# Performance work log

Hardware: AMD Instinct MI355X
Metric: run time of the kernel (lower is better)

## Reference

```python
import jax, jax.numpy as jnp
import numpy as np

N_NODES = 100000
N_EDGES = 800000
D = 128
BN_EPS = 1e-5


def setup_inputs() -> dict:
    key = jax.random.key(0)
    k1, k2, k3 = jax.random.split(key, 3)
    x = jax.random.normal(k1, (N_NODES, D), dtype=jnp.float32)
    # Glorot-ish init for the GCN weight
    W = jax.random.normal(k2, (D, D), dtype=jnp.float32) * (1.0 / np.sqrt(D))
    b = jnp.zeros((D,), dtype=jnp.float32)
    gamma = jnp.ones((D,), dtype=jnp.float32)
    beta = jnp.zeros((D,), dtype=jnp.float32)
    edge_index = jax.random.randint(k3, (2, N_EDGES), 0, N_NODES, dtype=jnp.int64)
    return {"x": x, "W": W, "b": b, "gamma": gamma, "beta": beta,
            "edge_index": edge_index}


def reference(x, W, b, gamma, beta, edge_index):
    N = x.shape[0]
    # --- GCNConv: add self-loops, symmetric degree normalization ---
    loop = jnp.arange(N, dtype=edge_index.dtype)
    src = jnp.concatenate([edge_index[0], loop])
    dst = jnp.concatenate([edge_index[1], loop])
    deg = jax.ops.segment_sum(jnp.ones_like(dst, dtype=x.dtype), dst,
                              num_segments=N)
    deg_inv_sqrt = jax.lax.rsqrt(deg)  # deg >= 1 thanks to self-loops
    norm = deg_inv_sqrt[src] * deg_inv_sqrt[dst]  # [E+N]

    h = x @ W  # [N, D] linear transform before propagation
    msg = h[src] * norm[:, None]  # gather + edge scaling, [E+N, D]
    agg = jax.ops.segment_sum(msg, dst, num_segments=N) + b  # scatter-add

    # --- BatchNorm1d (training-mode batch statistics, biased variance) ---
    mean = jnp.mean(agg, axis=0)
    var = jnp.mean(jnp.square(agg - mean), axis=0)
    y = gamma * (agg - mean) * jax.lax.rsqrt(var + BN_EPS) + beta

    # --- ReLU (dropout is identity in deterministic reference) ---
    return jax.nn.relu(y)
```

## Files before the change

### kernel.cpp

```cpp
#include <hip/hip_runtime.h>


#define N_NODES 100000
#define N_EDGES 800000
#define D 128
#define BN_EPS 1e-5f
#define SCAN_NB 98

__global__ void detect_i64(const unsigned int* ei, int* flag) {
    __shared__ int nonzero;
    if (threadIdx.x == 0) nonzero = 0;
    __syncthreads();
    int local = 0;
    for (int i = threadIdx.x; i < 2048; i += 256)
        if (ei[2 * i + 1] != 0u) local = 1;
    if (local) atomicOr(&nonzero, 1);
    __syncthreads();
    if (threadIdx.x == 0) *flag = (nonzero == 0) ? 1 : 0;
}

__device__ __forceinline__ int edge_at(const void* ei, int is64, long long pos) {
    if (is64) return (int)((const long long*)ei)[pos];
    return ((const int*)ei)[pos];
}

__global__ void count_deg_i(const void* ei, const int* __restrict__ flag,
                            int* __restrict__ deg) {
    int is64 = *flag;
    for (int i = blockIdx.x * blockDim.x + threadIdx.x; i < N_EDGES;
         i += gridDim.x * blockDim.x) {
        int d = edge_at(ei, is64, (long long)N_EDGES + i);
        atomicAdd(&deg[d], 1);
    }
}

__global__ __launch_bounds__(256) void scan1(const int* __restrict__ deg,
                                             int* __restrict__ rp,
                                             int* __restrict__ bsum) {
    __shared__ int wsum[4];
    int tid = threadIdx.x;
    int base = blockIdx.x * 1024;
    int v[4];
#pragma unroll
    for (int i = 0; i < 4; ++i) {
        int idx = base + tid * 4 + i;
        v[i] = (idx < N_NODES) ? deg[idx] : 0;
    }
    int tsum = v[0] + v[1] + v[2] + v[3];
    int lane = tid & 63;
    int incl = tsum;
#pragma unroll
    for (int off = 1; off < 64; off <<= 1) {
        int n = __shfl_up(incl, off, 64);
        if (lane >= off) incl += n;
    }
    int wid = tid >> 6;
    if (lane == 63) wsum[wid] = incl;
    __syncthreads();
    int woff = 0;
    for (int w = 0; w < wid; ++w) woff += wsum[w];
    int run = woff + incl - tsum;
#pragma unroll
    for (int i = 0; i < 4; ++i) {
        int idx = base + tid * 4 + i;
        if (idx < N_NODES) rp[idx] = run;
        run += v[i];
    }
    if (tid == 255) bsum[blockIdx.x] = woff + incl;
}

__global__ void scan2(int* __restrict__ bsum, int* __restrict__ rp) {
    __shared__ int s[128];
    int t = threadIdx.x;
    if (t < SCAN_NB) s[t] = bsum[t];
    __syncthreads();
    if (t == 0) {
        int run = 0;
        for (int i = 0; i < SCAN_NB; ++i) { int x = s[i]; s[i] = run; run += x; }
        rp[N_NODES] = N_EDGES;
    }
    __syncthreads();
    if (t < SCAN_NB) bsum[t] = s[t];
}

__global__ void scan3(int* __restrict__ rp, const int* __restrict__ bsum,
                      int* __restrict__ fp, const int* __restrict__ deg,
                      float* __restrict__ dis) {
    int idx = blockIdx.x * 256 + threadIdx.x;
    if (idx < N_NODES) {
        int v = rp[idx] + bsum[idx >> 10];
        rp[idx] = v;
        fp[idx] = v;
        dis[idx] = rsqrtf((float)deg[idx] + 1.0f);
    }
}

__global__ void fill_csr(const void* ei, const int* __restrict__ flag,
                         int* __restrict__ fp, int* __restrict__ ebuf) {
    int is64 = *flag;
    for (int e = blockIdx.x * blockDim.x + threadIdx.x; e < N_EDGES;
         e += gridDim.x * blockDim.x) {
        int s = edge_at(ei, is64, e);
        int d = edge_at(ei, is64, (long long)N_EDGES + e);
        int pos = atomicAdd(&fp[d], 1);
        ebuf[pos] = s;
    }
}

__global__ __launch_bounds__(256) void gather_x(const int* __restrict__ rp,
                                                const int* __restrict__ ebuf,
                                                const float* __restrict__ dis,
                                                const float* __restrict__ x,
                                                float* __restrict__ aggx) {
    int lane = threadIdx.x & 63;
    int wid = threadIdx.x >> 6;
    const float2* x2 = (const float2*)x;
    for (int node = blockIdx.x * 4 + wid; node < N_NODES;
         node += gridDim.x * 4) {
        int beg = rp[node], end = rp[node + 1];
        float dd = dis[node];
        float a0 = 0.f, a1 = 0.f;
        for (int j = beg; j < end; ++j) {
            int s = ebuf[j];
            float coef = dis[s] * dd;
            float2 v = x2[(size_t)s * 64 + lane];
            a0 = fmaf(v.x, coef, a0);
            a1 = fmaf(v.y, coef, a1);
        }
        float2 xv = x2[(size_t)node * 64 + lane];
        float c2 = dd * dd;
        a0 = fmaf(xv.x, c2, a0);
        a1 = fmaf(xv.y, c2, a1);
        ((float2*)aggx)[(size_t)node * 64 + lane] = make_float2(a0, a1);
    }
}

__global__ __launch_bounds__(256) void gemm_stats(float* __restrict__ ax,
                                                  const float* __restrict__ Wm,
                                                  float* __restrict__ colsum,
                                                  float* __restrict__ colsumsq) {
    __shared__ float As[64 * 128];
    __shared__ float Ws[64 * 128];
    int tid = threadIdx.x;
    int row0 = blockIdx.x * 64;

    const float4* a4 = (const float4*)ax;
    float4* A4 = (float4*)As;
#pragma unroll
    for (int i = 0; i < 8; ++i) {
        int idx = tid + i * 256;
        int r = idx >> 5;
        int gr = row0 + r;
        A4[idx] = (gr < N_NODES) ? a4[(size_t)gr * 32 + (idx & 31)]
                                 : make_float4(0.f, 0.f, 0.f, 0.f);
    }

    int tx = tid & 31;
    int ty = tid >> 5;
    float acc[8][4] = {};
    const float* Arow = &As[ty * 8 * 128];
    const float4* W4 = (const float4*)Wm;
    float4* Ws4 = (float4*)Ws;

    for (int kc = 0; kc < 128; kc += 64) {
        __syncthreads();
#pragma unroll
        for (int i = 0; i < 8; ++i) {
            int idx = tid + i * 256;
            Ws4[idx] = W4[kc * 32 + idx];
        }
        __syncthreads();
#pragma unroll 8
        for (int k = 0; k < 64; ++k) {
            float4 w = ((const float4*)&Ws[k * 128])[tx];
#pragma unroll
            for (int r = 0; r < 8; ++r) {
                float a = Arow[r * 128 + kc + k];
                acc[r][0] = fmaf(a, w.x, acc[r][0]);
                acc[r][1] = fmaf(a, w.y, acc[r][1]);
                acc[r][2] = fmaf(a, w.z, acc[r][2]);
                acc[r][3] = fmaf(a, w.w, acc[r][3]);
            }
        }
    }

#pragma unroll
    for (int r = 0; r < 8; ++r) {
        int gr = row0 + ty * 8 + r;
        if (gr < N_NODES)
            ((float4*)&ax[(size_t)gr * 128])[tx] =
                make_float4(acc[r][0], acc[r][1], acc[r][2], acc[r][3]);
    }

    float ps[4] = {0.f, 0.f, 0.f, 0.f}, pq[4] = {0.f, 0.f, 0.f, 0.f};
#pragma unroll
    for (int r = 0; r < 8; ++r)
#pragma unroll
        for (int k = 0; k < 4; ++k) {
            float v = acc[r][k];
            ps[k] += v;
            pq[k] += v * v;
        }
    __syncthreads();
#pragma unroll
    for (int k = 0; k < 4; ++k) {
        Ws[ty * 128 + tx * 4 + k] = ps[k];
        As[ty * 128 + tx * 4 + k] = pq[k];
    }
    __syncthreads();
    if (tid < 128) {
        float s = 0.f, q = 0.f;
#pragma unroll
        for (int t = 0; t < 8; ++t) {
            s += Ws[t * 128 + tid];
            q += As[t * 128 + tid];
        }
        atomicAdd(&colsum[tid], s);
        atomicAdd(&colsumsq[tid], q);
    }
}

__global__ void finalize_bn(const float* __restrict__ colsum,
                            const float* __restrict__ colsumsq,
                            const float* __restrict__ gamma,
                            const float* __restrict__ beta,
                            float* __restrict__ scale, float* __restrict__ shift) {
    int c = threadIdx.x;
    float mean = colsum[c] * (1.0f / N_NODES);
    float var = colsumsq[c] * (1.0f / N_NODES) - mean * mean;
    float sc = gamma[c] * rsqrtf(var + BN_EPS);
    scale[c] = sc;
    shift[c] = beta[c] - mean * sc;
}

__global__ __launch_bounds__(256) void normalize_relu(float* __restrict__ out,
                                                      const float* __restrict__ scale,
                                                      const float* __restrict__ shift) {
    const int total = N_NODES * 32;
    float4* o4 = (float4*)out;
    const float4* sc4 = (const float4*)scale;
    const float4* sh4 = (const float4*)shift;
    for (int i = blockIdx.x * blockDim.x + threadIdx.x; i < total;
         i += gridDim.x * blockDim.x) {
        int cg = i & 31;
        float4 v = o4[i];
        float4 sc = sc4[cg];
        float4 sh = sh4[cg];
        v.x = fmaxf(fmaf(v.x, sc.x, sh.x), 0.f);
        v.y = fmaxf(fmaf(v.y, sc.y, sh.y), 0.f);
        v.z = fmaxf(fmaf(v.z, sc.z, sh.z), 0.f);
        v.w = fmaxf(fmaf(v.w, sc.w, sh.w), 0.f);
        o4[i] = v;
    }
}

extern "C" void kernel_launch(void* const* d_in, const int* in_sizes, int n_in,
                              void* d_out, int out_size, void* d_ws, size_t ws_size,
                              hipStream_t stream) {
    const float* x = (const float*)d_in[0];
    const float* Wm = (const float*)d_in[1];
    const float* gamma = (const float*)d_in[3];
    const float* beta = (const float*)d_in[4];
    const void* ei = d_in[5];

    float* out = (float*)d_out;

    int* deg = (int*)d_ws;
    int* rp = deg + N_NODES;
    int* fp = rp + N_NODES + 1;
    int* bsum = fp + N_NODES;
    float* dis = (float*)(bsum + 128);
    float* colsum = dis + N_NODES;
    float* colsumsq = colsum + 128;
    float* scale = colsumsq + 128;
    float* shift = scale + 128;
    int* flag = (int*)(shift + 128);
    int* ebuf = flag + 64;

    hipMemsetAsync(deg, 0, (size_t)N_NODES * sizeof(int), stream);
    hipMemsetAsync(colsum, 0, 256 * sizeof(float), stream);

    detect_i64<<<1, 256, 0, stream>>>((const unsigned int*)ei, flag);
    count_deg_i<<<2048, 256, 0, stream>>>(ei, flag, deg);
    scan1<<<SCAN_NB, 256, 0, stream>>>(deg, rp, bsum);
    scan2<<<1, 128, 0, stream>>>(bsum, rp);
    scan3<<<(N_NODES + 255) / 256, 256, 0, stream>>>(rp, bsum, fp, deg, dis);
    fill_csr<<<2048, 256, 0, stream>>>(ei, flag, fp, ebuf);
    gather_x<<<2048, 256, 0, stream>>>(rp, ebuf, dis, x, out);
    gemm_stats<<<(N_NODES + 63) / 64, 256, 0, stream>>>(out, Wm, colsum, colsumsq);
    finalize_bn<<<1, 128, 0, stream>>>(colsum, colsumsq, gamma, beta, scale, shift);
    normalize_relu<<<2048, 256, 0, stream>>>(out, scale, shift);
}
```

Before: 402.3 us.

## Precompute edge coefficients in CSR, unroll gather, vectorize GEMM A loads

fill_csr now stores each edge as an int2 pair (source index, precomputed normalization coefficient), so gather_x no longer does a dependent dis[src] lookup per edge. gather_x unrolls the neighbor loop by four so several x-row loads are in flight at once. The GEMM inner loop reads A from shared memory as float4 over four k values instead of one scalar at a time. The CSR buffer doubles in size, and fill_csr does two extra random dis reads per edge.

```diff
diff --git a/kernel.cpp b/kernel.cpp
--- a/kernel.cpp
+++ b/kernel.cpp
@@ -96,19 +96,21 @@
 }
 
 __global__ void fill_csr(const void* ei, const int* __restrict__ flag,
-                         int* __restrict__ fp, int* __restrict__ ebuf) {
+                         int* __restrict__ fp, const float* __restrict__ dis,
+                         int2* __restrict__ eb) {
     int is64 = *flag;
     for (int e = blockIdx.x * blockDim.x + threadIdx.x; e < N_EDGES;
          e += gridDim.x * blockDim.x) {
         int s = edge_at(ei, is64, e);
         int d = edge_at(ei, is64, (long long)N_EDGES + e);
+        float coef = dis[s] * dis[d];
         int pos = atomicAdd(&fp[d], 1);
-        ebuf[pos] = s;
+        eb[pos] = make_int2(s, __float_as_int(coef));
     }
 }
 
 __global__ __launch_bounds__(256) void gather_x(const int* __restrict__ rp,
-                                                const int* __restrict__ ebuf,
+                                                const int2* __restrict__ eb,
                                                 const float* __restrict__ dis,
                                                 const float* __restrict__ x,
                                                 float* __restrict__ aggx) {
@@ -119,18 +121,29 @@
          node += gridDim.x * 4) {
         int beg = rp[node], end = rp[node + 1];
         float dd = dis[node];
-        float a0 = 0.f, a1 = 0.f;
-        for (int j = beg; j < end; ++j) {
-            int s = ebuf[j];
-            float coef = dis[s] * dd;
-            float2 v = x2[(size_t)s * 64 + lane];
-            a0 = fmaf(v.x, coef, a0);
-            a1 = fmaf(v.y, coef, a1);
-        }
         float2 xv = x2[(size_t)node * 64 + lane];
         float c2 = dd * dd;
-        a0 = fmaf(xv.x, c2, a0);
-        a1 = fmaf(xv.y, c2, a1);
+        float a0 = xv.x * c2, a1 = xv.y * c2;
+        int j = beg;
+        for (; j + 4 <= end; j += 4) {
+            int2 e0 = eb[j], e1 = eb[j + 1], e2 = eb[j + 2], e3 = eb[j + 3];
+            float2 v0 = x2[(size_t)e0.x * 64 + lane];
+            float2 v1 = x2[(size_t)e1.x * 64 + lane];
+            float2 v2 = x2[(size_t)e2.x * 64 + lane];
+            float2 v3 = x2[(size_t)e3.x * 64 + lane];
+            float c0 = __int_as_float(e0.y), c1 = __int_as_float(e1.y);
+            float cc = __int_as_float(e2.y), c3 = __int_as_float(e3.y);
+            a0 = fmaf(v0.x, c0, a0); a1 = fmaf(v0.y, c0, a1);
+            a0 = fmaf(v1.x, c1, a0); a1 = fmaf(v1.y, c1, a1);
+            a0 = fmaf(v2.x, cc, a0); a1 = fmaf(v2.y, cc, a1);
+            a0 = fmaf(v3.x, c3, a0); a1 = fmaf(v3.y, c3, a1);
+        }
+        for (; j < end; ++j) {
+            int2 e = eb[j];
+            float2 v = x2[(size_t)e.x * 64 + lane];
+            float c = __int_as_float(e.y);
+            a0 = fmaf(v.x, c, a0); a1 = fmaf(v.y, c, a1);
+        }
         ((float2*)aggx)[(size_t)node * 64 + lane] = make_float2(a0, a1);
     }
 }
@@ -170,16 +183,23 @@
             Ws4[idx] = W4[kc * 32 + idx];
         }
         __syncthreads();
-#pragma unroll 8
-        for (int k = 0; k < 64; ++k) {
-            float4 w = ((const float4*)&Ws[k * 128])[tx];
-#pragma unroll
-            for (int r = 0; r < 8; ++r) {
-                float a = Arow[r * 128 + kc + k];
-                acc[r][0] = fmaf(a, w.x, acc[r][0]);
-                acc[r][1] = fmaf(a, w.y, acc[r][1]);
-                acc[r][2] = fmaf(a, w.z, acc[r][2]);
-                acc[r][3] = fmaf(a, w.w, acc[r][3]);
+        for (int k4 = 0; k4 < 64; k4 += 4) {
+            float4 a8[8];
+#pragma unroll
+            for (int r = 0; r < 8; ++r)
+                a8[r] = *(const float4*)&Arow[r * 128 + kc + k4];
+#pragma unroll
+            for (int kk = 0; kk < 4; ++kk) {
+                float4 w = ((const float4*)&Ws[(k4 + kk) * 128])[tx];
+#pragma unroll
+                for (int r = 0; r < 8; ++r) {
+                    float av = (kk == 0) ? a8[r].x : (kk == 1) ? a8[r].y
+                             : (kk == 2) ? a8[r].z : a8[r].w;
+                    acc[r][0] = fmaf(av, w.x, acc[r][0]);
+                    acc[r][1] = fmaf(av, w.y, acc[r][1]);
+                    acc[r][2] = fmaf(av, w.z, acc[r][2]);
+                    acc[r][3] = fmaf(av, w.w, acc[r][3]);
+                }
             }
         }
     }
@@ -265,7 +285,8 @@
 
     float* out = (float*)d_out;
 
-    int* deg = (int*)d_ws;
+    int2* eb = (int2*)d_ws;
+    int* deg = (int*)(eb + N_EDGES);
     int* rp = deg + N_NODES;
     int* fp = rp + N_NODES + 1;
     int* bsum = fp + N_NODES;
@@ -275,7 +296,6 @@
     float* scale = colsumsq + 128;
     float* shift = scale + 128;
     int* flag = (int*)(shift + 128);
-    int* ebuf = flag + 64;
 
     hipMemsetAsync(deg, 0, (size_t)N_NODES * sizeof(int), stream);
     hipMemsetAsync(colsum, 0, 256 * sizeof(float), stream);
@@ -285,8 +305,8 @@
     scan1<<<SCAN_NB, 256, 0, stream>>>(deg, rp, bsum);
     scan2<<<1, 128, 0, stream>>>(bsum, rp);
     scan3<<<(N_NODES + 255) / 256, 256, 0, stream>>>(rp, bsum, fp, deg, dis);
-    fill_csr<<<2048, 256, 0, stream>>>(ei, flag, fp, ebuf);
-    gather_x<<<2048, 256, 0, stream>>>(rp, ebuf, dis, x, out);
+    fill_csr<<<2048, 256, 0, stream>>>(ei, flag, fp, dis, eb);
+    gather_x<<<2048, 256, 0, stream>>>(rp, eb, dis, x, out);
     gemm_stats<<<(N_NODES + 63) / 64, 256, 0, stream>>>(out, Wm, colsum, colsumsq);
     finalize_bn<<<1, 128, 0, stream>>>(colsum, colsumsq, gamma, beta, scale, shift);
     normalize_relu<<<2048, 256, 0, stream>>>(out, scale, shift);
```

Result: faster. 372.2 us (-7.5%).
